# Optimization experiments

Measured on AMD Instinct MI355X. Metric: run time of the kernel, lower is better.

## Reference

```python
import jax, jax.numpy as jnp
import numpy as np

E, N, R, H, D, O, L = 1600000, 50000, 6, 128, 256, 1, 3


def setup_inputs() -> dict:
    key = jax.random.key(0)
    ks = jax.random.split(key, 8)
    return {
        "x": jax.random.normal(ks[0], (E, H), jnp.float32),
        "rbf": jax.random.normal(ks[1], (E, R), jnp.float32),
        "i": jax.random.randint(ks[2], (E,), 0, N, dtype=jnp.int32),
        "W_rbf": jax.random.normal(ks[3], (H, R), jnp.float32) * 0.3,   # lin_rbf.weight (no bias)
        "W_up": jax.random.normal(ks[4], (D, H), jnp.float32) * 0.08,   # lin_up.weight
        "b_up": jnp.zeros((D,), jnp.float32),
        "Ws": jax.random.normal(ks[5], (L, D, D), jnp.float32) * 0.06,  # stacked lins weights
        "bs": jnp.zeros((L, D), jnp.float32),
        "W_out": jax.random.normal(ks[6], (O, D), jnp.float32) * 0.1,   # lin.weight (no bias)
        "num_nodes": N,
    }


def reference(x, rbf, i, W_rbf, W_up, b_up, Ws, bs, W_out, num_nodes):
    # edge gate: lin_rbf(rbf) * x  -> [E, H]
    g = (rbf @ W_rbf.T) * x
    # scatter-sum edges -> nodes  -> [N, H]
    h = jax.ops.segment_sum(g, i, num_segments=num_nodes)
    # lin_up  -> [N, D]
    h = h @ W_up.T + b_up
    # MLP stack with SiLU
    for l in range(Ws.shape[0]):
        h = jax.nn.silu(h @ Ws[l].T + bs[l])
    # final projection (no bias) -> [N, O]
    return h @ W_out.T
```

## Files before the change

### kernel.cpp

```cpp
#include <hip/hip_runtime.h>

#define NN     50000
#define HDIM   128
#define DDIM   256
#define RDIM   6
#define NLAYER 3
#define CAP    128

typedef short bf16x8 __attribute__((ext_vector_type(8)));
typedef float f32x4  __attribute__((ext_vector_type(4)));

__device__ __forceinline__ unsigned short f2bf(float f) {
    union { float f; unsigned int u; } v; v.f = f;
    unsigned int r = v.u + 0x7FFFu + ((v.u >> 16) & 1u);
    return (unsigned short)(r >> 16);
}

__global__ void prep_k(const float* __restrict__ Wup, const float* __restrict__ Ws,
                       unsigned short* __restrict__ wbup, unsigned short* __restrict__ wbs,
                       int* __restrict__ cnt) {
    int t = blockIdx.x * 256 + threadIdx.x;
    if (t < DDIM * HDIM) wbup[t] = f2bf(Wup[t]);
    if (t < NLAYER * DDIM * DDIM) wbs[t] = f2bf(Ws[t]);
    if (t < NN) cnt[t] = 0;
}

__global__ void bucket_k(const int* __restrict__ idx, int* __restrict__ cnt,
                         int* __restrict__ bucket, int E) {
    int t = blockIdx.x * 256 + threadIdx.x;
    if (t < E) {
        int n = idx[t];
        int p = atomicAdd(&cnt[n], 1);
        if (p < CAP) bucket[(long)n * CAP + p] = t;
    }
}

__device__ __forceinline__ void edge_acc(const float* __restrict__ x, const float* __restrict__ rbf,
                                         int e, int lane, const float* w0, const float* w1,
                                         float& a0, float& a1) {
    const float* rp = rbf + (long)e * RDIM;
    float2 r01 = *reinterpret_cast<const float2*>(rp);
    float2 r23 = *reinterpret_cast<const float2*>(rp + 2);
    float2 r45 = *reinterpret_cast<const float2*>(rp + 4);
    float2 xv  = *(reinterpret_cast<const float2*>(x + (long)e * HDIM) + lane);
    float s0 = w0[0] * r01.x + w0[1] * r01.y + w0[2] * r23.x +
               w0[3] * r23.y + w0[4] * r45.x + w0[5] * r45.y;
    float s1 = w1[0] * r01.x + w1[1] * r01.y + w1[2] * r23.x +
               w1[3] * r23.y + w1[4] * r45.x + w1[5] * r45.y;
    a0 += s0 * xv.x; a1 += s1 * xv.y;
}

__global__ __launch_bounds__(256) void gather_k(
        const float* __restrict__ x, const float* __restrict__ rbf,
        const float* __restrict__ Wrbf, const int* __restrict__ cnt,
        const int* __restrict__ bucket, unsigned short* __restrict__ h0, int n_nodes) {
    int wid = threadIdx.x >> 6, lane = threadIdx.x & 63;
    int n = blockIdx.x * 4 + wid;
    if (n >= n_nodes) return;

    int hA = 2 * lane;
    float w0[RDIM], w1[RDIM];
#pragma unroll
    for (int r = 0; r < RDIM; ++r) {
        w0[r] = Wrbf[hA * RDIM + r];
        w1[r] = Wrbf[(hA + 1) * RDIM + r];
    }

    int c = cnt[n]; if (c > CAP) c = CAP;
    const int* brow = bucket + (long)n * CAP;
    float a0 = 0.f, a1 = 0.f;
    int j = 0;
    for (; j + 8 <= c; j += 8) {
        int4 eA = *reinterpret_cast<const int4*>(brow + j);
        int4 eB = *reinterpret_cast<const int4*>(brow + j + 4);
        int e0 = __builtin_amdgcn_readfirstlane(eA.x);
        int e1 = __builtin_amdgcn_readfirstlane(eA.y);
        int e2 = __builtin_amdgcn_readfirstlane(eA.z);
        int e3 = __builtin_amdgcn_readfirstlane(eA.w);
        int e4 = __builtin_amdgcn_readfirstlane(eB.x);
        int e5 = __builtin_amdgcn_readfirstlane(eB.y);
        int e6 = __builtin_amdgcn_readfirstlane(eB.z);
        int e7 = __builtin_amdgcn_readfirstlane(eB.w);
        edge_acc(x, rbf, e0, lane, w0, w1, a0, a1);
        edge_acc(x, rbf, e1, lane, w0, w1, a0, a1);
        edge_acc(x, rbf, e2, lane, w0, w1, a0, a1);
        edge_acc(x, rbf, e3, lane, w0, w1, a0, a1);
        edge_acc(x, rbf, e4, lane, w0, w1, a0, a1);
        edge_acc(x, rbf, e5, lane, w0, w1, a0, a1);
        edge_acc(x, rbf, e6, lane, w0, w1, a0, a1);
        edge_acc(x, rbf, e7, lane, w0, w1, a0, a1);
    }
    for (; j < c; ++j) {
        int e = __builtin_amdgcn_readfirstlane(brow[j]);
        edge_acc(x, rbf, e, lane, w0, w1, a0, a1);
    }

    unsigned int packed = (unsigned int)f2bf(a0) | ((unsigned int)f2bf(a1) << 16);
    *reinterpret_cast<unsigned int*>(h0 + (long)n * HDIM + hA) = packed;
}

template <int K>
__device__ __forceinline__ bf16x8 lds_afrag(const unsigned short* buf, int mi, int kk, int lr, int q) {
    int row = mi * 16 + lr;
    int byte = row * (2 * K) + (((kk * 64 + q * 16)) ^ ((row & 7) << 4));
    return *reinterpret_cast<const bf16x8*>((const char*)buf + byte);
}

template <int K, bool SILU, bool FINAL>
__device__ __forceinline__ void layer_compute(
        const unsigned short* Abuf, const unsigned short* __restrict__ W,
        const float* __restrict__ bias, unsigned short* Obuf,
        const float* __restrict__ Wout, float* partialRow, int lane, int w) {
    int lr = lane & 15, q = lane >> 4;
    int cb = w * 64;

    f32x4 acc[4][4];
#pragma unroll
    for (int mi = 0; mi < 4; ++mi)
#pragma unroll
        for (int ni = 0; ni < 4; ++ni) acc[mi][ni] = (f32x4){0.f, 0.f, 0.f, 0.f};

    const unsigned short* bptr[4];
#pragma unroll
    for (int ni = 0; ni < 4; ++ni) bptr[ni] = W + (long)(cb + ni * 16 + lr) * K + q * 8;

#pragma unroll
    for (int kk = 0; kk < K / 32; ++kk) {
        bf16x8 af[4], bfr[4];
#pragma unroll
        for (int mi = 0; mi < 4; ++mi) af[mi] = lds_afrag<K>(Abuf, mi, kk, lr, q);
#pragma unroll
        for (int ni = 0; ni < 4; ++ni) bfr[ni] = *reinterpret_cast<const bf16x8*>(bptr[ni] + kk * 32);
#pragma unroll
        for (int mi = 0; mi < 4; ++mi)
#pragma unroll
            for (int ni = 0; ni < 4; ++ni)
                acc[mi][ni] = __builtin_amdgcn_mfma_f32_16x16x32_bf16(af[mi], bfr[ni], acc[mi][ni], 0, 0, 0);
    }

    float bv[4];
#pragma unroll
    for (int ni = 0; ni < 4; ++ni) bv[ni] = bias[cb + ni * 16 + lr];

    if (!FINAL) {
#pragma unroll
        for (int mi = 0; mi < 4; ++mi)
#pragma unroll
            for (int ni = 0; ni < 4; ++ni) {
                int col = cb + ni * 16 + lr;
#pragma unroll
                for (int jj = 0; jj < 4; ++jj) {
                    int row = mi * 16 + q * 4 + jj;
                    float v = acc[mi][ni][jj] + bv[ni];
                    if (SILU) v = v / (1.f + __expf(-v));
                    int byte = row * 512 + ((2 * col) ^ ((row & 7) << 4));
                    *reinterpret_cast<unsigned short*>((char*)Obuf + byte) = f2bf(v);
                }
            }
    } else {
        float wo[4];
#pragma unroll
        for (int ni = 0; ni < 4; ++ni) wo[ni] = Wout[cb + ni * 16 + lr];
#pragma unroll
        for (int mi = 0; mi < 4; ++mi)
#pragma unroll
            for (int jj = 0; jj < 4; ++jj) {
                float s = 0.f;
#pragma unroll
                for (int ni = 0; ni < 4; ++ni) {
                    float v = acc[mi][ni][jj] + bv[ni];
                    v = v / (1.f + __expf(-v));
                    s += v * wo[ni];
                }
                s += __shfl_xor(s, 1, 64);
                s += __shfl_xor(s, 2, 64);
                s += __shfl_xor(s, 4, 64);
                s += __shfl_xor(s, 8, 64);
                if (lr == 0) partialRow[mi * 16 + q * 4 + jj] = s;
            }
    }
}

__global__ __launch_bounds__(256) void mlp_fused_k(
        const unsigned short* __restrict__ h0,
        const unsigned short* __restrict__ wbup, const float* __restrict__ bup,
        const unsigned short* __restrict__ wbs, const float* __restrict__ bs,
        const float* __restrict__ Wout, float* __restrict__ out, int M) {
    __shared__ unsigned short regA[64 * 256];
    __shared__ unsigned short regB[64 * 256];
    __shared__ float partial[4][64];

    int tid = threadIdx.x, lane = tid & 63, w = tid >> 6;
    long rbase = (long)blockIdx.x * 64;

#pragma unroll
    for (int s = 0; s < 4; ++s) {
        int idx = s * 256 + tid;
        int row = idx >> 4, ch = idx & 15;
        bf16x8 v = *reinterpret_cast<const bf16x8*>(h0 + (rbase + row) * HDIM + ch * 8);
        int byte = row * 256 + ((ch * 16) ^ ((row & 7) << 4));
        *reinterpret_cast<bf16x8*>((char*)regA + byte) = v;
    }
    __syncthreads();

    layer_compute<HDIM, false, false>(regA, wbup, bup, regB, nullptr, nullptr, lane, w);
    __syncthreads();
    layer_compute<DDIM, true,  false>(regB, wbs + 0 * DDIM * DDIM, bs + 0 * DDIM, regA, nullptr, nullptr, lane, w);
    __syncthreads();
    layer_compute<DDIM, true,  false>(regA, wbs + 1 * DDIM * DDIM, bs + 1 * DDIM, regB, nullptr, nullptr, lane, w);
    __syncthreads();
    layer_compute<DDIM, true,  true >(regB, wbs + 2 * DDIM * DDIM, bs + 2 * DDIM, nullptr, Wout, &partial[w][0], lane, w);
    __syncthreads();

    if (tid < 64) {
        long row = rbase + tid;
        if (row < M)
            out[row] = partial[0][tid] + partial[1][tid] + partial[2][tid] + partial[3][tid];
    }
}

extern "C" void kernel_launch(void* const* d_in, const int* in_sizes, int n_in,
                              void* d_out, int out_size, void* d_ws, size_t ws_size,
                              hipStream_t stream) {
    const float* x    = (const float*)d_in[0];
    const float* rbf  = (const float*)d_in[1];
    const int*   idx  = (const int*)d_in[2];
    const float* Wrbf = (const float*)d_in[3];
    const float* Wup  = (const float*)d_in[4];
    const float* bup  = (const float*)d_in[5];
    const float* Ws   = (const float*)d_in[6];
    const float* bs   = (const float*)d_in[7];
    const float* Wout = (const float*)d_in[8];
    const int E = in_sizes[2];
    const int N = NN;
    const int mtiles = (N + 63) / 64;
    const int MPAD = mtiles * 64;

    char* ws = (char*)d_ws;
    size_t off = 0;
    auto alloc = [&](size_t bytes) -> void* {
        void* p = ws + off;
        off += (bytes + 255) & ~(size_t)255;
        return p;
    };
    int* cnt    = (int*)alloc((size_t)N * 4);
    int* bucket = (int*)alloc((size_t)N * CAP * 4);
    unsigned short* h0   = (unsigned short*)alloc((size_t)MPAD * HDIM * 2);
    unsigned short* wbup = (unsigned short*)alloc((size_t)DDIM * HDIM * 2);
    unsigned short* wbs  = (unsigned short*)alloc((size_t)NLAYER * DDIM * DDIM * 2);
    (void)ws_size; (void)n_in; (void)out_size;

    prep_k<<<(NLAYER * DDIM * DDIM + 255) / 256, 256, 0, stream>>>(Wup, Ws, wbup, wbs, cnt);
    bucket_k<<<(E + 255) / 256, 256, 0, stream>>>(idx, cnt, bucket, E);
    gather_k<<<(N + 3) / 4, 256, 0, stream>>>(x, rbf, Wrbf, cnt, bucket, h0, N);
    mlp_fused_k<<<mtiles, 256, 0, stream>>>(h0, wbup, bup, wbs, bs, Wout, (float*)d_out, N);
}
```

Baseline: 399.9 us.

## Fuse the edge gather into the MLP kernel and drop the h0 buffer

The separate gather kernel is removed. Each 64-row MLP block now gathers its own nodes, each wave handling 16 nodes one after another, and writes the bf16 aggregated features straight into swizzled LDS. This avoids writing and re-reading the h0 intermediate in global memory and saves one kernel launch. In exchange the bandwidth-bound gather now runs at the occupancy of the LDS-heavy MLP kernel, which allows far fewer waves in flight per CU. That can reduce memory-level parallelism for the irregular edge loads.

```diff
diff --git a/kernel.cpp b/kernel.cpp
--- a/kernel.cpp
+++ b/kernel.cpp
@@ -50,55 +50,6 @@
     a0 += s0 * xv.x; a1 += s1 * xv.y;
 }
 
-__global__ __launch_bounds__(256) void gather_k(
-        const float* __restrict__ x, const float* __restrict__ rbf,
-        const float* __restrict__ Wrbf, const int* __restrict__ cnt,
-        const int* __restrict__ bucket, unsigned short* __restrict__ h0, int n_nodes) {
-    int wid = threadIdx.x >> 6, lane = threadIdx.x & 63;
-    int n = blockIdx.x * 4 + wid;
-    if (n >= n_nodes) return;
-
-    int hA = 2 * lane;
-    float w0[RDIM], w1[RDIM];
-#pragma unroll
-    for (int r = 0; r < RDIM; ++r) {
-        w0[r] = Wrbf[hA * RDIM + r];
-        w1[r] = Wrbf[(hA + 1) * RDIM + r];
-    }
-
-    int c = cnt[n]; if (c > CAP) c = CAP;
-    const int* brow = bucket + (long)n * CAP;
-    float a0 = 0.f, a1 = 0.f;
-    int j = 0;
-    for (; j + 8 <= c; j += 8) {
-        int4 eA = *reinterpret_cast<const int4*>(brow + j);
-        int4 eB = *reinterpret_cast<const int4*>(brow + j + 4);
-        int e0 = __builtin_amdgcn_readfirstlane(eA.x);
-        int e1 = __builtin_amdgcn_readfirstlane(eA.y);
-        int e2 = __builtin_amdgcn_readfirstlane(eA.z);
-        int e3 = __builtin_amdgcn_readfirstlane(eA.w);
-        int e4 = __builtin_amdgcn_readfirstlane(eB.x);
-        int e5 = __builtin_amdgcn_readfirstlane(eB.y);
-        int e6 = __builtin_amdgcn_readfirstlane(eB.z);
-        int e7 = __builtin_amdgcn_readfirstlane(eB.w);
-        edge_acc(x, rbf, e0, lane, w0, w1, a0, a1);
-        edge_acc(x, rbf, e1, lane, w0, w1, a0, a1);
-        edge_acc(x, rbf, e2, lane, w0, w1, a0, a1);
-        edge_acc(x, rbf, e3, lane, w0, w1, a0, a1);
-        edge_acc(x, rbf, e4, lane, w0, w1, a0, a1);
-        edge_acc(x, rbf, e5, lane, w0, w1, a0, a1);
-        edge_acc(x, rbf, e6, lane, w0, w1, a0, a1);
-        edge_acc(x, rbf, e7, lane, w0, w1, a0, a1);
-    }
-    for (; j < c; ++j) {
-        int e = __builtin_amdgcn_readfirstlane(brow[j]);
-        edge_acc(x, rbf, e, lane, w0, w1, a0, a1);
-    }
-
-    unsigned int packed = (unsigned int)f2bf(a0) | ((unsigned int)f2bf(a1) << 16);
-    *reinterpret_cast<unsigned int*>(h0 + (long)n * HDIM + hA) = packed;
-}
-
 template <int K>
 __device__ __forceinline__ bf16x8 lds_afrag(const unsigned short* buf, int mi, int kk, int lr, int q) {
     int row = mi * 16 + lr;
@@ -181,8 +132,10 @@
     }
 }
 
-__global__ __launch_bounds__(256) void mlp_fused_k(
-        const unsigned short* __restrict__ h0,
+__global__ __launch_bounds__(256) void node_k(
+        const float* __restrict__ x, const float* __restrict__ rbf,
+        const float* __restrict__ Wrbf, const int* __restrict__ cnt,
+        const int* __restrict__ bucket,
         const unsigned short* __restrict__ wbup, const float* __restrict__ bup,
         const unsigned short* __restrict__ wbs, const float* __restrict__ bs,
         const float* __restrict__ Wout, float* __restrict__ out, int M) {
@@ -193,13 +146,49 @@
     int tid = threadIdx.x, lane = tid & 63, w = tid >> 6;
     long rbase = (long)blockIdx.x * 64;
 
-#pragma unroll
-    for (int s = 0; s < 4; ++s) {
-        int idx = s * 256 + tid;
-        int row = idx >> 4, ch = idx & 15;
-        bf16x8 v = *reinterpret_cast<const bf16x8*>(h0 + (rbase + row) * HDIM + ch * 8);
-        int byte = row * 256 + ((ch * 16) ^ ((row & 7) << 4));
-        *reinterpret_cast<bf16x8*>((char*)regA + byte) = v;
+    float w0[RDIM], w1[RDIM];
+#pragma unroll
+    for (int r = 0; r < RDIM; ++r) {
+        w0[r] = Wrbf[(2 * lane) * RDIM + r];
+        w1[r] = Wrbf[(2 * lane + 1) * RDIM + r];
+    }
+
+    for (int t = 0; t < 16; ++t) {
+        int ln = w * 16 + t;
+        long n = rbase + ln;
+        float a0 = 0.f, a1 = 0.f;
+        if (n < M) {
+            int c = cnt[n]; if (c > CAP) c = CAP;
+            const int* brow = bucket + n * CAP;
+            int j = 0;
+            for (; j + 8 <= c; j += 8) {
+                int4 eA = *reinterpret_cast<const int4*>(brow + j);
+                int4 eB = *reinterpret_cast<const int4*>(brow + j + 4);
+                int e0 = __builtin_amdgcn_readfirstlane(eA.x);
+                int e1 = __builtin_amdgcn_readfirstlane(eA.y);
+                int e2 = __builtin_amdgcn_readfirstlane(eA.z);
+                int e3 = __builtin_amdgcn_readfirstlane(eA.w);
+                int e4 = __builtin_amdgcn_readfirstlane(eB.x);
+                int e5 = __builtin_amdgcn_readfirstlane(eB.y);
+                int e6 = __builtin_amdgcn_readfirstlane(eB.z);
+                int e7 = __builtin_amdgcn_readfirstlane(eB.w);
+                edge_acc(x, rbf, e0, lane, w0, w1, a0, a1);
+                edge_acc(x, rbf, e1, lane, w0, w1, a0, a1);
+                edge_acc(x, rbf, e2, lane, w0, w1, a0, a1);
+                edge_acc(x, rbf, e3, lane, w0, w1, a0, a1);
+                edge_acc(x, rbf, e4, lane, w0, w1, a0, a1);
+                edge_acc(x, rbf, e5, lane, w0, w1, a0, a1);
+                edge_acc(x, rbf, e6, lane, w0, w1, a0, a1);
+                edge_acc(x, rbf, e7, lane, w0, w1, a0, a1);
+            }
+            for (; j < c; ++j) {
+                int e = __builtin_amdgcn_readfirstlane(brow[j]);
+                edge_acc(x, rbf, e, lane, w0, w1, a0, a1);
+            }
+        }
+        unsigned int packed = (unsigned int)f2bf(a0) | ((unsigned int)f2bf(a1) << 16);
+        int byte = ln * 256 + ((4 * lane) ^ ((ln & 7) << 4));
+        *reinterpret_cast<unsigned int*>((char*)regA + byte) = packed;
     }
     __syncthreads();
 
@@ -234,7 +223,6 @@
     const int E = in_sizes[2];
     const int N = NN;
     const int mtiles = (N + 63) / 64;
-    const int MPAD = mtiles * 64;
 
     char* ws = (char*)d_ws;
     size_t off = 0;
@@ -245,13 +233,12 @@
     };
     int* cnt    = (int*)alloc((size_t)N * 4);
     int* bucket = (int*)alloc((size_t)N * CAP * 4);
-    unsigned short* h0   = (unsigned short*)alloc((size_t)MPAD * HDIM * 2);
     unsigned short* wbup = (unsigned short*)alloc((size_t)DDIM * HDIM * 2);
     unsigned short* wbs  = (unsigned short*)alloc((size_t)NLAYER * DDIM * DDIM * 2);
     (void)ws_size; (void)n_in; (void)out_size;
 
     prep_k<<<(NLAYER * DDIM * DDIM + 255) / 256, 256, 0, stream>>>(Wup, Ws, wbup, wbs, cnt);
     bucket_k<<<(E + 255) / 256, 256, 0, stream>>>(idx, cnt, bucket, E);
-    gather_k<<<(N + 3) / 4, 256, 0, stream>>>(x, rbf, Wrbf, cnt, bucket, h0, N);
-    mlp_fused_k<<<mtiles, 256, 0, stream>>>(h0, wbup, bup, wbs, bs, Wout, (float*)d_out, N);
-}
+    node_k<<<mtiles, 256, 0, stream>>>(x, rbf, Wrbf, cnt, bucket,
+                                       wbup, bup, wbs, bs, Wout, (float*)d_out, N);
+}
```

New measurement: 548.8 us. 37.2% more time.

## Use a single in-place LDS activation buffer and raise launch-bounds occupancy hint

Applied to the files above, without the earlier changes.

The fused MLP kernel now keeps one 32KB shared buffer instead of two ping-pong buffers. Each layer's results stay in registers until a barrier, then overwrite the buffer in place, which takes one extra __syncthreads per layer. Launch bounds now request 4 blocks per CU to raise occupancy, and both LDS use and register budget are tightened toward that target. The risks are register spills under the new bound and the extra barriers, which serialize the MFMA and store phases within each block.

```diff
diff --git a/kernel.cpp b/kernel.cpp
--- a/kernel.cpp
+++ b/kernel.cpp
@@ -106,92 +106,102 @@
     return *reinterpret_cast<const bf16x8*>((const char*)buf + byte);
 }
 
-template <int K, bool SILU, bool FINAL>
-__device__ __forceinline__ void layer_compute(
+template <int K>
+__device__ __forceinline__ void layer_mfma(
         const unsigned short* Abuf, const unsigned short* __restrict__ W,
-        const float* __restrict__ bias, unsigned short* Obuf,
+        f32x4 (&acc)[4][4], int lane, int w) {
+    int lr = lane & 15, q = lane >> 4;
+    int cb = w * 64;
+#pragma unroll
+    for (int mi = 0; mi < 4; ++mi)
+#pragma unroll
+        for (int ni = 0; ni < 4; ++ni) acc[mi][ni] = (f32x4){0.f, 0.f, 0.f, 0.f};
+
+    const unsigned short* bptr[4];
+#pragma unroll
+    for (int ni = 0; ni < 4; ++ni) bptr[ni] = W + (long)(cb + ni * 16 + lr) * K + q * 8;
+
+#pragma unroll
+    for (int kk = 0; kk < K / 32; ++kk) {
+        bf16x8 af[4], bfr[4];
+#pragma unroll
+        for (int mi = 0; mi < 4; ++mi) af[mi] = lds_afrag<K>(Abuf, mi, kk, lr, q);
+#pragma unroll
+        for (int ni = 0; ni < 4; ++ni) bfr[ni] = *reinterpret_cast<const bf16x8*>(bptr[ni] + kk * 32);
+#pragma unroll
+        for (int mi = 0; mi < 4; ++mi)
+#pragma unroll
+            for (int ni = 0; ni < 4; ++ni)
+                acc[mi][ni] = __builtin_amdgcn_mfma_f32_16x16x32_bf16(af[mi], bfr[ni], acc[mi][ni], 0, 0, 0);
+    }
+}
+
+template <bool SILU>
+__device__ __forceinline__ void layer_store(
+        unsigned short* Obuf, f32x4 (&acc)[4][4],
+        const float* __restrict__ bias, int lane, int w) {
+    int lr = lane & 15, q = lane >> 4;
+    int cb = w * 64;
+    float bv[4];
+#pragma unroll
+    for (int ni = 0; ni < 4; ++ni) bv[ni] = bias[cb + ni * 16 + lr];
+#pragma unroll
+    for (int mi = 0; mi < 4; ++mi)
+#pragma unroll
+        for (int ni = 0; ni < 4; ++ni) {
+            int col = cb + ni * 16 + lr;
+#pragma unroll
+            for (int jj = 0; jj < 4; ++jj) {
+                int row = mi * 16 + q * 4 + jj;
+                float v = acc[mi][ni][jj] + bv[ni];
+                if (SILU) v = v / (1.f + __expf(-v));
+                int byte = row * 512 + ((2 * col) ^ ((row & 7) << 4));
+                *reinterpret_cast<unsigned short*>((char*)Obuf + byte) = f2bf(v);
+            }
+        }
+}
+
+__device__ __forceinline__ void layer_final(
+        f32x4 (&acc)[4][4], const float* __restrict__ bias,
         const float* __restrict__ Wout, float* partialRow, int lane, int w) {
     int lr = lane & 15, q = lane >> 4;
     int cb = w * 64;
-
-    f32x4 acc[4][4];
+    float bv[4], wo[4];
+#pragma unroll
+    for (int ni = 0; ni < 4; ++ni) {
+        bv[ni] = bias[cb + ni * 16 + lr];
+        wo[ni] = Wout[cb + ni * 16 + lr];
+    }
 #pragma unroll
     for (int mi = 0; mi < 4; ++mi)
 #pragma unroll
-        for (int ni = 0; ni < 4; ++ni) acc[mi][ni] = (f32x4){0.f, 0.f, 0.f, 0.f};
-
-    const unsigned short* bptr[4];
-#pragma unroll
-    for (int ni = 0; ni < 4; ++ni) bptr[ni] = W + (long)(cb + ni * 16 + lr) * K + q * 8;
-
-#pragma unroll
-    for (int kk = 0; kk < K / 32; ++kk) {
-        bf16x8 af[4], bfr[4];
-#pragma unroll
-        for (int mi = 0; mi < 4; ++mi) af[mi] = lds_afrag<K>(Abuf, mi, kk, lr, q);
-#pragma unroll
-        for (int ni = 0; ni < 4; ++ni) bfr[ni] = *reinterpret_cast<const bf16x8*>(bptr[ni] + kk * 32);
-#pragma unroll
-        for (int mi = 0; mi < 4; ++mi)
-#pragma unroll
-            for (int ni = 0; ni < 4; ++ni)
-                acc[mi][ni] = __builtin_amdgcn_mfma_f32_16x16x32_bf16(af[mi], bfr[ni], acc[mi][ni], 0, 0, 0);
-    }
-
-    float bv[4];
-#pragma unroll
-    for (int ni = 0; ni < 4; ++ni) bv[ni] = bias[cb + ni * 16 + lr];
-
-    if (!FINAL) {
-#pragma unroll
-        for (int mi = 0; mi < 4; ++mi)
+        for (int jj = 0; jj < 4; ++jj) {
+            float s = 0.f;
 #pragma unroll
             for (int ni = 0; ni < 4; ++ni) {
-                int col = cb + ni * 16 + lr;
-#pragma unroll
-                for (int jj = 0; jj < 4; ++jj) {
-                    int row = mi * 16 + q * 4 + jj;
-                    float v = acc[mi][ni][jj] + bv[ni];
-                    if (SILU) v = v / (1.f + __expf(-v));
-                    int byte = row * 512 + ((2 * col) ^ ((row & 7) << 4));
-                    *reinterpret_cast<unsigned short*>((char*)Obuf + byte) = f2bf(v);
-                }
+                float v = acc[mi][ni][jj] + bv[ni];
+                v = v / (1.f + __expf(-v));
+                s += v * wo[ni];
             }
-    } else {
-        float wo[4];
-#pragma unroll
-        for (int ni = 0; ni < 4; ++ni) wo[ni] = Wout[cb + ni * 16 + lr];
-#pragma unroll
-        for (int mi = 0; mi < 4; ++mi)
-#pragma unroll
-            for (int jj = 0; jj < 4; ++jj) {
-                float s = 0.f;
-#pragma unroll
-                for (int ni = 0; ni < 4; ++ni) {
-                    float v = acc[mi][ni][jj] + bv[ni];
-                    v = v / (1.f + __expf(-v));
-                    s += v * wo[ni];
-                }
-                s += __shfl_xor(s, 1, 64);
-                s += __shfl_xor(s, 2, 64);
-                s += __shfl_xor(s, 4, 64);
-                s += __shfl_xor(s, 8, 64);
-                if (lr == 0) partialRow[mi * 16 + q * 4 + jj] = s;
-            }
-    }
-}
-
-__global__ __launch_bounds__(256) void mlp_fused_k(
+            s += __shfl_xor(s, 1, 64);
+            s += __shfl_xor(s, 2, 64);
+            s += __shfl_xor(s, 4, 64);
+            s += __shfl_xor(s, 8, 64);
+            if (lr == 0) partialRow[mi * 16 + q * 4 + jj] = s;
+        }
+}
+
+__global__ __launch_bounds__(256, 4) void mlp_fused_k(
         const unsigned short* __restrict__ h0,
         const unsigned short* __restrict__ wbup, const float* __restrict__ bup,
         const unsigned short* __restrict__ wbs, const float* __restrict__ bs,
         const float* __restrict__ Wout, float* __restrict__ out, int M) {
-    __shared__ unsigned short regA[64 * 256];
-    __shared__ unsigned short regB[64 * 256];
+    __shared__ unsigned short buf[64 * 256];
     __shared__ float partial[4][64];
 
     int tid = threadIdx.x, lane = tid & 63, w = tid >> 6;
     long rbase = (long)blockIdx.x * 64;
+    f32x4 acc[4][4];
 
 #pragma unroll
     for (int s = 0; s < 4; ++s) {
@@ -199,17 +209,24 @@
         int row = idx >> 4, ch = idx & 15;
         bf16x8 v = *reinterpret_cast<const bf16x8*>(h0 + (rbase + row) * HDIM + ch * 8);
         int byte = row * 256 + ((ch * 16) ^ ((row & 7) << 4));
-        *reinterpret_cast<bf16x8*>((char*)regA + byte) = v;
-    }
-    __syncthreads();
-
-    layer_compute<HDIM, false, false>(regA, wbup, bup, regB, nullptr, nullptr, lane, w);
-    __syncthreads();
-    layer_compute<DDIM, true,  false>(regB, wbs + 0 * DDIM * DDIM, bs + 0 * DDIM, regA, nullptr, nullptr, lane, w);
-    __syncthreads();
-    layer_compute<DDIM, true,  false>(regA, wbs + 1 * DDIM * DDIM, bs + 1 * DDIM, regB, nullptr, nullptr, lane, w);
-    __syncthreads();
-    layer_compute<DDIM, true,  true >(regB, wbs + 2 * DDIM * DDIM, bs + 2 * DDIM, nullptr, Wout, &partial[w][0], lane, w);
+        *reinterpret_cast<bf16x8*>((char*)buf + byte) = v;
+    }
+    __syncthreads();
+
+    layer_mfma<HDIM>(buf, wbup, acc, lane, w);
+    __syncthreads();
+    layer_store<false>(buf, acc, bup, lane, w);
+    __syncthreads();
+    layer_mfma<DDIM>(buf, wbs + 0 * DDIM * DDIM, acc, lane, w);
+    __syncthreads();
+    layer_store<true>(buf, acc, bs + 0 * DDIM, lane, w);
+    __syncthreads();
+    layer_mfma<DDIM>(buf, wbs + 1 * DDIM * DDIM, acc, lane, w);
+    __syncthreads();
+    layer_store<true>(buf, acc, bs + 1 * DDIM, lane, w);
+    __syncthreads();
+    layer_mfma<DDIM>(buf, wbs + 2 * DDIM * DDIM, acc, lane, w);
+    layer_final(acc, bs + 2 * DDIM, Wout, &partial[w][0], lane, w);
     __syncthreads();
 
     if (tid < 64) {
```

Measured after the change: 425.3 us. 6.3% more time.
